# Optimization experiments

Hardware: AMD Instinct MI355X
Metric: run time of the kernel (lower is better)

Reference implementation:

```python
import jax, jax.numpy as jnp
import numpy as np

B, S, DM, H, SD = 8, 2048, 512, 8, 64
INNER = H * SD
HID = 4 * DM
EPS = 1e-5


def setup_inputs() -> dict:
    key = jax.random.key(0)
    ks = jax.random.split(key, 12)
    p = lambda k, sh: jax.random.normal(k, sh, dtype=jnp.float32) * 0.02
    return {
        "x": jax.random.normal(ks[0], (B, S, DM), dtype=jnp.float32),
        "norm_g": jnp.ones((DM,), jnp.float32),
        "norm_b": jnp.zeros((DM,), jnp.float32),
        "ffn_norm_g": jnp.ones((DM,), jnp.float32),
        "ffn_norm_b": jnp.zeros((DM,), jnp.float32),
        "Wa": p(ks[1], (INNER, DM)),
        "Wb": p(ks[2], (INNER, DM)),
        "Wql": p(ks[3], (INNER, DM)),
        "Wqr": p(ks[4], (INNER, DM)),
        "Wsd": p(ks[5], (H, DM)),
        "bsd": jnp.zeros((H,), jnp.float32),
        "Wpd": p(ks[6], (H, DM)),
        "bpd": jnp.zeros((H,), jnp.float32),
        "Wout": p(ks[7], (DM, INNER)),
        "W1": p(ks[8], (HID, DM)),
        "b1": jnp.zeros((HID,), jnp.float32),
        "W2": p(ks[9], (DM, HID)),
        "b2": jnp.zeros((DM,), jnp.float32),
    }


def _ln(x, g, b):
    m = x.mean(-1, keepdims=True)
    v = ((x - m) ** 2).mean(-1, keepdims=True)
    return (x - m) / jnp.sqrt(v + EPS) * g + b


def reference(x, norm_g, norm_b, ffn_norm_g, ffn_norm_b, Wa, Wb, Wql, Wqr,
              Wsd, bsd, Wpd, bpd, Wout, W1, b1, W2, b2):
    n = _ln(x, norm_g, norm_b)  # [B,S,DM]
    # project, reshape to heads, move time axis first for scan: [S,B,H,SD]
    tm = lambda t: t.reshape(B, S, H, SD).transpose(1, 0, 2, 3)
    a_all = tm(jnp.tanh(n @ Wa.T))
    b_all = tm(jnp.tanh(n @ Wb.T))
    ql_all = tm(jnp.tanh(n @ Wql.T))
    qr_all = tm(jnp.tanh(n @ Wqr.T))
    sd_all = jax.nn.sigmoid(n @ Wsd.T + bsd).transpose(1, 0, 2)[..., None]        # [S,B,H,1]
    pd_all = jax.nn.sigmoid(n @ Wpd.T + bpd).transpose(1, 0, 2)[..., None, None]  # [S,B,H,1,1]

    def step(carry, inp):
        state, pair = carry  # state [B,H,SD], pair [B,H,SD,SD]
        at, bt, qlt, sdt, pdt = inp
        prev = state
        state = sdt * state + (1.0 - sdt) * at
        pair = pdt * pair + (1.0 - pdt) * jnp.einsum('bhd,bhe->bhde', prev, bt)
        lc = jnp.einsum('bhde,bhd->bhe', pair, qlt)  # left context [B,H,SD]
        return (state, pair), lc

    init = (jnp.zeros((B, H, SD), x.dtype), jnp.zeros((B, H, SD, SD), x.dtype))
    _, lc = jax.lax.scan(step, init, (a_all, b_all, ql_all, sd_all, pd_all))  # [S,B,H,SD]

    mixed = ((lc * qr_all).transpose(1, 0, 2, 3).reshape(B, S, INNER)) @ Wout.T  # [B,S,DM]
    r = x + mixed  # dropout is identity in eval
    h = jax.nn.gelu(_ln(r, ffn_norm_g, ffn_norm_b) @ W1.T + b1, approximate=False)
    return r + h @ W2.T + b2
```

## Files before the change

kernel.cpp:

```cpp
#include <hip/hip_runtime.h>
#include <cstdint>
#include <cstddef>

#define B_    8
#define S_    2048
#define DM_   512
#define H_    8
#define SD_   64
#define HID_  2048
#define ROWS  (B_*S_)
#define BH    (B_*H_)
#define NCHUNK 32
#define CLEN   64
#define EPS_  1e-5f

typedef __bf16 bf16x8 __attribute__((ext_vector_type(8)));
typedef float  floatx4 __attribute__((ext_vector_type(4)));

static __device__ __forceinline__ float bf2f(unsigned short h){
  union { unsigned int u; float f; } v; v.u = ((unsigned int)h) << 16; return v.f;
}
static __device__ __forceinline__ unsigned short f2bf(float f){
  union { float f; unsigned int u; } v; v.f = f;
  unsigned int r = v.u + 0x7fffu + ((v.u >> 16) & 1u);
  return (unsigned short)(r >> 16);
}
static __device__ __forceinline__ float fast_tanh(float x){
  float ax = fabsf(x);
  float e  = __expf(2.f*ax);
  float t  = 1.f - 2.f/(e+1.f);
  return copysignf(t, x);
}
static __device__ __forceinline__ float sigmoidf_(float z){
  return 1.f/(1.f + expf(-z));
}
static __device__ __forceinline__ float gelu_exact(float x){
  return 0.5f*x*(1.f + erff(x*0.70710678118654752440f));
}
static __device__ __forceinline__ void gld_lds16(const unsigned short* g, unsigned short* lds){
  __builtin_amdgcn_global_load_lds(
      (const __attribute__((address_space(1))) void*)g,
      (__attribute__((address_space(3))) void*)lds,
      16, 0, 0);
}
static __device__ __forceinline__ int swz(int row, int col){
  return row*64 + (((col>>3) ^ (row&7))<<3) + (col&7);
}

__global__ __launch_bounds__(256) void cvt_weights(
    const float* __restrict__ wa, const float* __restrict__ wb,
    const float* __restrict__ wql, const float* __restrict__ wqr,
    const float* __restrict__ wout, const float* __restrict__ w1,
    const float* __restrict__ w2,
    unsigned short* __restrict__ wcat, unsigned short* __restrict__ woutb,
    unsigned short* __restrict__ w1b, unsigned short* __restrict__ w2b){
  int i = blockIdx.x*256 + threadIdx.x;
  const float* s; unsigned short* d; int base;
  if      (i <  65536){ s=wa;   d=wcat;          base=i; }
  else if (i < 131072){ s=wb;   d=wcat+262144;   base=i-65536; }
  else if (i < 196608){ s=wql;  d=wcat+524288;   base=i-131072; }
  else if (i < 262144){ s=wqr;  d=wcat+786432;   base=i-196608; }
  else if (i < 327680){ s=wout; d=woutb;         base=i-262144; }
  else if (i < 589824){ s=w1;   d=w1b;           base=i-327680; }
  else                { s=w2;   d=w2b;           base=i-589824; }
  float4 v = ((const float4*)s)[base];
  ushort4 o; o.x=f2bf(v.x); o.y=f2bf(v.y); o.z=f2bf(v.z); o.w=f2bf(v.w);
  ((ushort4*)d)[base] = o;
}

__global__ __launch_bounds__(64) void ln_gates(
    const float* __restrict__ x, const float* __restrict__ gam, const float* __restrict__ bet,
    const float* __restrict__ Wsd, const float* __restrict__ bsd,
    const float* __restrict__ Wpd, const float* __restrict__ bpd,
    unsigned short* __restrict__ nbf, float* __restrict__ sdo, float* __restrict__ pdo){
  const int row = blockIdx.x, l = threadIdx.x;
  const float* xr = x + (size_t)row*DM_;
  float4 v0 = ((const float4*)xr)[l*2];
  float4 v1 = ((const float4*)xr)[l*2+1];
  float v[8] = {v0.x,v0.y,v0.z,v0.w,v1.x,v1.y,v1.z,v1.w};
  float s = 0.f;
  #pragma unroll
  for (int i=0;i<8;++i) s += v[i];
  #pragma unroll
  for (int m=1;m<64;m<<=1) s += __shfl_xor(s, m);
  const float mean = s * (1.f/512.f);
  float q = 0.f;
  #pragma unroll
  for (int i=0;i<8;++i){ float d = v[i]-mean; q += d*d; }
  #pragma unroll
  for (int m=1;m<64;m<<=1) q += __shfl_xor(q, m);
  const float rstd = rsqrtf(q*(1.f/512.f) + EPS_);
  float4 g0 = ((const float4*)gam)[l*2], g1 = ((const float4*)gam)[l*2+1];
  float4 b0 = ((const float4*)bet)[l*2], b1 = ((const float4*)bet)[l*2+1];
  float gg[8] = {g0.x,g0.y,g0.z,g0.w,g1.x,g1.y,g1.z,g1.w};
  float bb[8] = {b0.x,b0.y,b0.z,b0.w,b1.x,b1.y,b1.z,b1.w};
  float n[8];
  #pragma unroll
  for (int i=0;i<8;++i) n[i] = (v[i]-mean)*rstd*gg[i] + bb[i];
  ushort4 o0, o1;
  o0.x=f2bf(n[0]); o0.y=f2bf(n[1]); o0.z=f2bf(n[2]); o0.w=f2bf(n[3]);
  o1.x=f2bf(n[4]); o1.y=f2bf(n[5]); o1.z=f2bf(n[6]); o1.w=f2bf(n[7]);
  ((ushort4*)(nbf + (size_t)row*DM_))[l*2]   = o0;
  ((ushort4*)(nbf + (size_t)row*DM_))[l*2+1] = o1;
  float acc[16];
  #pragma unroll
  for (int hh=0; hh<8; ++hh){
    const float4* ws = (const float4*)(Wsd + hh*DM_) + l*2;
    const float4* wp = (const float4*)(Wpd + hh*DM_) + l*2;
    float4 a0=ws[0], a1=ws[1], p0=wp[0], p1=wp[1];
    acc[hh]   = n[0]*a0.x+n[1]*a0.y+n[2]*a0.z+n[3]*a0.w+n[4]*a1.x+n[5]*a1.y+n[6]*a1.z+n[7]*a1.w;
    acc[8+hh] = n[0]*p0.x+n[1]*p0.y+n[2]*p0.z+n[3]*p0.w+n[4]*p1.x+n[5]*p1.y+n[6]*p1.z+n[7]*p1.w;
  }
  #pragma unroll
  for (int k=0;k<16;++k){
    float a = acc[k];
    #pragma unroll
    for (int m=1;m<64;m<<=1) a += __shfl_xor(a, m);
    acc[k] = a;
  }
  if (l==0){
    #pragma unroll
    for (int hh=0; hh<8; ++hh){
      sdo[row*8+hh] = sigmoidf_(acc[hh]   + bsd[hh]);
      pdo[row*8+hh] = sigmoidf_(acc[8+hh] + bpd[hh]);
    }
  }
}

__global__ __launch_bounds__(64) void ln_plain(
    const unsigned short* __restrict__ xb, const float* __restrict__ gam, const float* __restrict__ bet,
    unsigned short* __restrict__ ob){
  const int row = blockIdx.x, l = threadIdx.x;
  const unsigned short* xr = xb + (size_t)row*DM_ + l*8;
  ushort4 u0 = *(const ushort4*)xr;
  ushort4 u1 = *(const ushort4*)(xr+4);
  float v[8] = {bf2f(u0.x),bf2f(u0.y),bf2f(u0.z),bf2f(u0.w),
                bf2f(u1.x),bf2f(u1.y),bf2f(u1.z),bf2f(u1.w)};
  float s = 0.f;
  #pragma unroll
  for (int i=0;i<8;++i) s += v[i];
  #pragma unroll
  for (int m=1;m<64;m<<=1) s += __shfl_xor(s, m);
  const float mean = s * (1.f/512.f);
  float q = 0.f;
  #pragma unroll
  for (int i=0;i<8;++i){ float d = v[i]-mean; q += d*d; }
  #pragma unroll
  for (int m=1;m<64;m<<=1) q += __shfl_xor(q, m);
  const float rstd = rsqrtf(q*(1.f/512.f) + EPS_);
  float4 g0 = ((const float4*)gam)[l*2], g1 = ((const float4*)gam)[l*2+1];
  float4 b0 = ((const float4*)bet)[l*2], b1 = ((const float4*)bet)[l*2+1];
  float gg[8] = {g0.x,g0.y,g0.z,g0.w,g1.x,g1.y,g1.z,g1.w};
  float bb[8] = {b0.x,b0.y,b0.z,b0.w,b1.x,b1.y,b1.z,b1.w};
  ushort4 o0, o1;
  o0.x=f2bf((v[0]-mean)*rstd*gg[0]+bb[0]); o0.y=f2bf((v[1]-mean)*rstd*gg[1]+bb[1]);
  o0.z=f2bf((v[2]-mean)*rstd*gg[2]+bb[2]); o0.w=f2bf((v[3]-mean)*rstd*gg[3]+bb[3]);
  o1.x=f2bf((v[4]-mean)*rstd*gg[4]+bb[4]); o1.y=f2bf((v[5]-mean)*rstd*gg[5]+bb[5]);
  o1.z=f2bf((v[6]-mean)*rstd*gg[6]+bb[6]); o1.w=f2bf((v[7]-mean)*rstd*gg[7]+bb[7]);
  ((ushort4*)(ob + (size_t)row*DM_))[l*2]   = o0;
  ((ushort4*)(ob + (size_t)row*DM_))[l*2+1] = o1;
}

template<int MODE>
__global__ __launch_bounds__(256) void gemm128(
    const unsigned short* __restrict__ A, const unsigned short* __restrict__ W,
    const float* __restrict__ bias, const float* __restrict__ residf,
    const unsigned short* __restrict__ residb,
    float* __restrict__ outf, unsigned short* __restrict__ outb,
    int N, int K){
  __shared__ __align__(16) unsigned short As[128*64];
  __shared__ __align__(16) unsigned short Ws[128*64];
  const int tid  = threadIdx.x;
  const int w    = tid >> 6;
  const int lane = tid & 63;
  const int mblk = blockIdx.x, nblk = blockIdx.y;
  const int mrow = (w >> 1) * 64;
  const int ncol = (w & 1) * 64;
  const int fr = lane & 15, fq = lane >> 4;

  int srow[4], scol[4];
  #pragma unroll
  for (int q=0;q<4;++q){
    const int p = q*256 + w*64 + lane;
    srow[q] = p >> 3;
    scol[q] = ((p & 7) ^ (srow[q] & 7)) * 8;
  }

  floatx4 acc[4][4];
  #pragma unroll
  for (int i=0;i<4;++i)
    #pragma unroll
    for (int j=0;j<4;++j)
      acc[i][j] = (floatx4){0.f,0.f,0.f,0.f};

  for (int k0=0; k0<K; k0+=64){
    #pragma unroll
    for (int q=0;q<4;++q){
      gld_lds16(A + (size_t)(mblk*128 + srow[q])*K + k0 + scol[q], As + (q*256 + w*64)*8);
      gld_lds16(W + (size_t)(nblk*128 + srow[q])*K + k0 + scol[q], Ws + (q*256 + w*64)*8);
    }
    __syncthreads();
    #pragma unroll
    for (int kh=0;kh<2;++kh){
      bf16x8 af[4], bf[4];
      #pragma unroll
      for (int i=0;i<4;++i) af[i] = *(const bf16x8*)&As[swz(mrow + i*16 + fr, kh*32 + fq*8)];
      #pragma unroll
      for (int j=0;j<4;++j) bf[j] = *(const bf16x8*)&Ws[swz(ncol + j*16 + fr, kh*32 + fq*8)];
      #pragma unroll
      for (int i=0;i<4;++i)
        #pragma unroll
        for (int j=0;j<4;++j)
          acc[i][j] = __builtin_amdgcn_mfma_f32_16x16x32_bf16(af[i], bf[j], acc[i][j], 0, 0, 0);
    }
    __syncthreads();
  }

  #pragma unroll
  for (int i=0;i<4;++i){
    const int grow_base = mblk*128 + mrow + i*16 + fq*4;
    #pragma unroll
    for (int j=0;j<4;++j){
      const int gcol = nblk*128 + ncol + j*16 + fr;
      float bias_v = 0.f;
      if (MODE==2 || MODE==3) bias_v = bias[gcol];
      #pragma unroll
      for (int r=0;r<4;++r){
        const size_t o = (size_t)(grow_base + r)*N + gcol;
        float v = acc[i][j][r];
        if      (MODE==0) outb[o] = f2bf(fast_tanh(v));
        else if (MODE==1) outb[o] = f2bf(residf[o] + v);
        else if (MODE==2) outb[o] = f2bf(gelu_exact(v + bias_v));
        else              outf[o] = bf2f(residb[o]) + v + bias_v;
      }
    }
  }
}

template<int MODE>
__global__ __launch_bounds__(256) void gemm128db(
    const unsigned short* __restrict__ A, const unsigned short* __restrict__ W,
    unsigned short* __restrict__ outb, int N, int K){
  __shared__ __align__(16) unsigned short As[2][128*64];
  __shared__ __align__(16) unsigned short Ws[2][128*64];
  const int tid  = threadIdx.x;
  const int w    = tid >> 6;
  const int lane = tid & 63;
  const int mblk = blockIdx.x, nblk = blockIdx.y;
  const int mrow = (w >> 1) * 64;
  const int ncol = (w & 1) * 64;
  const int fr = lane & 15, fq = lane >> 4;

  int srow[4], scol[4];
  #pragma unroll
  for (int q=0;q<4;++q){
    const int p = q*256 + w*64 + lane;
    srow[q] = p >> 3;
    scol[q] = ((p & 7) ^ (srow[q] & 7)) * 8;
  }

  floatx4 acc[4][4];
  #pragma unroll
  for (int i=0;i<4;++i)
    #pragma unroll
    for (int j=0;j<4;++j)
      acc[i][j] = (floatx4){0.f,0.f,0.f,0.f};

  #pragma unroll
  for (int q=0;q<4;++q){
    gld_lds16(A + (size_t)(mblk*128 + srow[q])*K + scol[q], As[0] + (q*256 + w*64)*8);
    gld_lds16(W + (size_t)(nblk*128 + srow[q])*K + scol[q], Ws[0] + (q*256 + w*64)*8);
  }

  const int nk = K >> 6;
  for (int it=0; it<nk; ++it){
    const int cur = it & 1;
    __syncthreads();
    if (it+1 < nk){
      const int k1 = (it+1) << 6;
      #pragma unroll
      for (int q=0;q<4;++q){
        gld_lds16(A + (size_t)(mblk*128 + srow[q])*K + k1 + scol[q], As[1-cur] + (q*256 + w*64)*8);
        gld_lds16(W + (size_t)(nblk*128 + srow[q])*K + k1 + scol[q], Ws[1-cur] + (q*256 + w*64)*8);
      }
    }
    #pragma unroll
    for (int kh=0;kh<2;++kh){
      bf16x8 af[4], bf[4];
      #pragma unroll
      for (int i=0;i<4;++i) af[i] = *(const bf16x8*)&As[cur][swz(mrow + i*16 + fr, kh*32 + fq*8)];
      #pragma unroll
      for (int j=0;j<4;++j) bf[j] = *(const bf16x8*)&Ws[cur][swz(ncol + j*16 + fr, kh*32 + fq*8)];
      #pragma unroll
      for (int i=0;i<4;++i)
        #pragma unroll
        for (int j=0;j<4;++j)
          acc[i][j] = __builtin_amdgcn_mfma_f32_16x16x32_bf16(af[i], bf[j], acc[i][j], 0, 0, 0);
    }
  }

  #pragma unroll
  for (int i=0;i<4;++i){
    const int grow_base = mblk*128 + mrow + i*16 + fq*4;
    #pragma unroll
    for (int j=0;j<4;++j){
      const int gcol = nblk*128 + ncol + j*16 + fr;
      #pragma unroll
      for (int r=0;r<4;++r){
        const size_t o = (size_t)(grow_base + r)*N + gcol;
        outb[o] = f2bf(fast_tanh(acc[i][j][r]));
      }
    }
  }
}

__global__ __launch_bounds__(64) void state_local(
    const unsigned short* __restrict__ proj, const float* __restrict__ sdo,
    unsigned short* __restrict__ slocb, float* __restrict__ Sarr,
    float* __restrict__ sEnd){
  const int c = blockIdx.x, bh = blockIdx.y, b = bh>>3, h = bh&7, d = threadIdx.x;
  float s = 0.f, S = 1.f;
  const int t0 = c*CLEN;
  #pragma unroll 4
  for (int j=0;j<CLEN;++j){
    const int t = t0 + j;
    float a  = bf2f(proj[((size_t)(b*S_+t))*2048 + h*64 + d]);
    float sv = sdo[(b*S_+t)*8 + h];
    s = sv*s + (1.f-sv)*a;
    S *= sv;
    slocb[((size_t)bh*S_ + t)*64 + d] = f2bf(s);
    if (d==0) Sarr[bh*S_ + t] = S;
  }
  sEnd[((size_t)c*BH + bh)*64 + d] = s;
}

__global__ __launch_bounds__(64) void state_combine(
    const float* __restrict__ sEnd, const float* __restrict__ Sarr,
    float* __restrict__ sinit){
  const int bh = blockIdx.x, d = threadIdx.x;
  float acc = 0.f;
  for (int c=0;c<NCHUNK;++c){
    sinit[((size_t)c*BH + bh)*64 + d] = acc;
    const int te = c*CLEN + CLEN - 1;
    acc = Sarr[bh*S_ + te]*acc + sEnd[((size_t)c*BH + bh)*64 + d];
  }
}

__global__ __launch_bounds__(256) void prev_mat(
    const unsigned short* __restrict__ slocb, const float* __restrict__ Sarr,
    const float* __restrict__ sinit, unsigned short* __restrict__ prevb){
  const size_t idx = (size_t)blockIdx.x*256 + threadIdx.x;
  const int d  = (int)(idx & 63);
  const size_t bt = idx >> 6;
  const int t  = (int)(bt & (S_-1));
  const int bh = (int)(bt >> 11);
  const int c = t >> 6, j = t & 63;
  float init = sinit[((size_t)c*BH + bh)*64 + d];
  float p;
  if (j==0) p = init;
  else {
    const size_t pt = (size_t)bh*S_ + (t-1);
    p = Sarr[pt]*init + bf2f(slocb[pt*64 + d]);
  }
  prevb[idx] = f2bf(p);
}

__global__ __launch_bounds__(64) void pair_localm(
    const unsigned short* __restrict__ proj, const float* __restrict__ pdo,
    const unsigned short* __restrict__ prevb, float* __restrict__ pairbuf,
    float* __restrict__ Dprod){
  __shared__ __align__(16) unsigned short Bt[4096];
  __shared__ __align__(16) unsigned short Pt[4096];
  const int c=blockIdx.x, bh=blockIdx.y, b=bh>>3, h=bh&7, l=threadIdx.x;
  const int t = c*CLEN + l;
  float pd = pdo[(b*S_+t)*8 + h];
  float D = pd;
  #pragma unroll
  for (int m=1;m<64;m<<=1){ float o = __shfl_up(D, m); if (l>=m) D *= o; }
  const float Dend = __shfl(D, 63);
  const float cu = (Dend / D) * (1.f - pd);
  if (l==63) Dprod[c*BH+bh] = Dend;
  {
    const unsigned short* brow = proj  + ((size_t)(b*S_+t))*2048 + 512 + h*64;
    const unsigned short* prow = prevb + ((size_t)bh*S_ + t)*64;
    #pragma unroll
    for (int e8=0;e8<8;++e8){
      ushort4 u0 = *(const ushort4*)(brow + e8*8);
      ushort4 u1 = *(const ushort4*)(brow + e8*8 + 4);
      unsigned short vs[8] = {u0.x,u0.y,u0.z,u0.w,u1.x,u1.y,u1.z,u1.w};
      ushort4 p0 = *(const ushort4*)(prow + e8*8);
      ushort4 p1 = *(const ushort4*)(prow + e8*8 + 4);
      unsigned short ps[8] = {p0.x,p0.y,p0.z,p0.w,p1.x,p1.y,p1.z,p1.w};
      #pragma unroll
      for (int q=0;q<8;++q){
        const int r = e8*8+q;
        Bt[swz(r, l)] = f2bf(cu * bf2f(vs[q]));
        Pt[swz(r, l)] = ps[q];
      }
    }
  }
  __syncthreads();
  const int fr = l & 15, fq = l >> 4;
  floatx4 acc[4][4];
  #pragma unroll
  for (int i=0;i<4;++i)
    #pragma unroll
    for (int j=0;j<4;++j) acc[i][j] = (floatx4){0.f,0.f,0.f,0.f};
  #pragma unroll
  for (int kh=0;kh<2;++kh){
    bf16x8 af[4], bfr[4];
    #pragma unroll
    for (int i=0;i<4;++i) af[i]  = *(const bf16x8*)&Bt[swz(i*16+fr, kh*32+fq*8)];
    #pragma unroll
    for (int j=0;j<4;++j) bfr[j] = *(const bf16x8*)&Pt[swz(j*16+fr, kh*32+fq*8)];
    #pragma unroll
    for (int i=0;i<4;++i)
      #pragma unroll
      for (int j=0;j<4;++j)
        acc[i][j] = __builtin_amdgcn_mfma_f32_16x16x32_bf16(af[i], bfr[j], acc[i][j], 0, 0, 0);
  }
  float* outp = pairbuf + ((size_t)c*BH + bh)*4096;
  #pragma unroll
  for (int i=0;i<4;++i)
    #pragma unroll
    for (int j=0;j<4;++j)
      #pragma unroll
      for (int r=0;r<4;++r)
        outp[(i*16+fq*4+r)*64 + j*16+fr] = acc[i][j][r];
}

__global__ __launch_bounds__(256) void pair_combine(
    float* __restrict__ pairbuf, const float* __restrict__ Dprod){
  const int idx = blockIdx.x*256 + threadIdx.x;
  const int de = idx & 4095, bh = idx >> 12;
  float acc = 0.f;
  for (int c=0;c<NCHUNK;++c){
    const size_t o = ((size_t)c*BH + bh)*4096 + de;
    float loc = pairbuf[o];
    pairbuf[o] = acc;
    acc = Dprod[c*BH + bh]*acc + loc;
  }
}

__global__ __launch_bounds__(64) void pair_finalm(
    const unsigned short* __restrict__ proj, const float* __restrict__ pdo,
    const unsigned short* __restrict__ prevb, const float* __restrict__ pinit,
    unsigned short* __restrict__ lcqr){
  __shared__ __align__(16) unsigned short Bt[4096];
  __shared__ __align__(16) unsigned short Tb[4096];
  __shared__ __align__(16) float Dtl[64];
  __shared__ __align__(16) float cudl[64];
  const int c=blockIdx.x, bh=blockIdx.y, b=bh>>3, h=bh&7, l=threadIdx.x;
  const int t0 = c*CLEN;
  const int trow = t0 + l;
  float pd = pdo[(b*S_+trow)*8 + h];
  float D = pd;
  #pragma unroll
  for (int m=1;m<64;m<<=1){ float o = __shfl_up(D, m); if (l>=m) D *= o; }
  Dtl[l]  = D;
  cudl[l] = (1.f - pd) / D;
  {
    const unsigned short* brow = proj + ((size_t)(b*S_+trow))*2048 + 512 + h*64;
    #pragma unroll
    for (int e8=0;e8<8;++e8){
      ushort4 u0 = *(const ushort4*)(brow + e8*8);
      ushort4 u1 = *(const ushort4*)(brow + e8*8 + 4);
      unsigned short vs[8] = {u0.x,u0.y,u0.z,u0.w,u1.x,u1.y,u1.z,u1.w};
      #pragma unroll
      for (int q=0;q<8;++q) Bt[swz(e8*8+q, l)] = vs[q];
    }
  }
  __syncthreads();
  const int fr = l & 15, fq = l >> 4;
  bf16x8 qf[4][2], pf[4][2];
  #pragma unroll
  for (int i=0;i<4;++i)
    #pragma unroll
    for (int kh=0;kh<2;++kh){
      qf[i][kh] = *(const bf16x8*)(proj  + ((size_t)(b*S_ + t0 + i*16 + fr))*2048 + 1024 + h*64 + kh*32 + fq*8);
      pf[i][kh] = *(const bf16x8*)(prevb + ((size_t)(bh*S_ + t0 + i*16 + fr))*64  + kh*32 + fq*8);
    }
  floatx4 sacc[4][4];
  #pragma unroll
  for (int i=0;i<4;++i)
    #pragma unroll
    for (int j=0;j<4;++j) sacc[i][j] = (floatx4){0.f,0.f,0.f,0.f};
  #pragma unroll
  for (int kh=0;kh<2;++kh)
    #pragma unroll
    for (int i=0;i<4;++i)
      #pragma unroll
      for (int j=0;j<4;++j)
        sacc[i][j] = __builtin_amdgcn_mfma_f32_16x16x32_bf16(qf[i][kh], pf[j][kh], sacc[i][j], 0, 0, 0);
  float mycud[4];
  #pragma unroll
  for (int j=0;j<4;++j) mycud[j] = cudl[j*16+fr];
  #pragma unroll
  for (int i=0;i<4;++i){
    floatx4 dtv = *(const floatx4*)&Dtl[i*16+fq*4];
    #pragma unroll
    for (int j=0;j<4;++j){
      const int uu = j*16+fr;
      #pragma unroll
      for (int r=0;r<4;++r){
        const int tt = i*16+fq*4+r;
        float v = (uu<=tt) ? (sacc[i][j][r]*dtv[r])*mycud[j] : 0.f;
        Tb[swz(tt, uu)] = f2bf(v);
      }
    }
  }
  __syncthreads();
  floatx4 acc[4][4];
  #pragma unroll
  for (int i=0;i<4;++i)
    #pragma unroll
    for (int j=0;j<4;++j) acc[i][j] = (floatx4){0.f,0.f,0.f,0.f};
  #pragma unroll
  for (int kh=0;kh<2;++kh){
    bf16x8 af[4], bfr[4];
    #pragma unroll
    for (int i=0;i<4;++i) af[i]  = *(const bf16x8*)&Tb[swz(i*16+fr, kh*32+fq*8)];
    #pragma unroll
    for (int j=0;j<4;++j) bfr[j] = *(const bf16x8*)&Bt[swz(j*16+fr, kh*32+fq*8)];
    #pragma unroll
    for (int i=0;i<4;++i)
      #pragma unroll
      for (int j=0;j<4;++j)
        acc[i][j] = __builtin_amdgcn_mfma_f32_16x16x32_bf16(af[i], bfr[j], acc[i][j], 0, 0, 0);
  }
  {
    const float* ibase = pinit + ((size_t)c*BH + bh)*4096;
    #pragma unroll
    for (int kh=0;kh<2;++kh){
      bf16x8 qs[4], inf[4];
      #pragma unroll
      for (int i=0;i<4;++i){
        const float sc = Dtl[i*16+fr];
        #pragma unroll
        for (int e=0;e<8;++e) qs[i][e] = (__bf16)(sc * (float)qf[i][kh][e]);
      }
      #pragma unroll
      for (int j=0;j<4;++j){
        const float* ip = ibase + (j*16+fr)*64 + kh*32 + fq*8;
        float4 f0 = *(const float4*)ip;
        float4 f1 = *(const float4*)(ip+4);
        inf[j][0]=(__bf16)f0.x; inf[j][1]=(__bf16)f0.y; inf[j][2]=(__bf16)f0.z; inf[j][3]=(__bf16)f0.w;
        inf[j][4]=(__bf16)f1.x; inf[j][5]=(__bf16)f1.y; inf[j][6]=(__bf16)f1.z; inf[j][7]=(__bf16)f1.w;
      }
      #pragma unroll
      for (int i=0;i<4;++i)
        #pragma unroll
        for (int j=0;j<4;++j)
          acc[i][j] = __builtin_amdgcn_mfma_f32_16x16x32_bf16(qs[i], inf[j], acc[i][j], 0, 0, 0);
    }
  }
  __syncthreads();
  #pragma unroll
  for (int i=0;i<4;++i)
    #pragma unroll
    for (int j=0;j<4;++j)
      #pragma unroll
      for (int r=0;r<4;++r)
        Tb[swz(i*16+fq*4+r, j*16+fr)] = f2bf(acc[i][j][r]);
  __syncthreads();
  {
    const unsigned short* qrow = proj + ((size_t)(b*S_+trow))*2048 + 1536 + h*64;
    unsigned short* orow = lcqr + ((size_t)(b*S_+trow))*512 + h*64;
    #pragma unroll
    for (int e8=0;e8<8;++e8){
      bf16x8 lcv = *(const bf16x8*)&Tb[swz(l, e8*8)];
      ushort4 q0 = *(const ushort4*)(qrow + e8*8);
      ushort4 q1 = *(const ushort4*)(qrow + e8*8 + 4);
      unsigned short qv[8] = {q0.x,q0.y,q0.z,q0.w,q1.x,q1.y,q1.z,q1.w};
      ushort4 o0, o1;
      o0.x = f2bf((float)lcv[0]*bf2f(qv[0]));
      o0.y = f2bf((float)lcv[1]*bf2f(qv[1]));
      o0.z = f2bf((float)lcv[2]*bf2f(qv[2]));
      o0.w = f2bf((float)lcv[3]*bf2f(qv[3]));
      o1.x = f2bf((float)lcv[4]*bf2f(qv[4]));
      o1.y = f2bf((float)lcv[5]*bf2f(qv[5]));
      o1.z = f2bf((float)lcv[6]*bf2f(qv[6]));
      o1.w = f2bf((float)lcv[7]*bf2f(qv[7]));
      *(ushort4*)(orow + e8*8)     = o0;
      *(ushort4*)(orow + e8*8 + 4) = o1;
    }
  }
}

extern "C" void kernel_launch(void* const* d_in, const int* in_sizes, int n_in,
                              void* d_out, int out_size, void* d_ws, size_t ws_size,
                              hipStream_t stream){
  (void)in_sizes; (void)n_in; (void)out_size; (void)ws_size;
  const float* x    = (const float*)d_in[0];
  const float* ng   = (const float*)d_in[1];
  const float* nb   = (const float*)d_in[2];
  const float* fng  = (const float*)d_in[3];
  const float* fnb  = (const float*)d_in[4];
  const float* Wa   = (const float*)d_in[5];
  const float* Wb   = (const float*)d_in[6];
  const float* Wql  = (const float*)d_in[7];
  const float* Wqr  = (const float*)d_in[8];
  const float* Wsd  = (const float*)d_in[9];
  const float* bsd  = (const float*)d_in[10];
  const float* Wpd  = (const float*)d_in[11];
  const float* bpd  = (const float*)d_in[12];
  const float* Wout = (const float*)d_in[13];
  const float* W1   = (const float*)d_in[14];
  const float* b1   = (const float*)d_in[15];
  const float* W2   = (const float*)d_in[16];
  const float* b2   = (const float*)d_in[17];
  float* out = (float*)d_out;
  char* ws = (char*)d_ws;

  size_t off = 0;
  auto alloc = [&](size_t bytes)->char*{ char* p = ws + off; off += (bytes + 255) & ~(size_t)255; return p; };
  char* RA = alloc((size_t)ROWS*DM_*2);
  char* RB = alloc((size_t)ROWS*2048*2);
  char* RD = alloc((size_t)BH*S_*64*4);
  char* RE = alloc((size_t)BH*S_*64*4);
  float* sdo   = (float*)alloc((size_t)ROWS*8*4);
  float* pdo   = (float*)alloc((size_t)ROWS*8*4);
  float* Sarr  = (float*)alloc((size_t)BH*S_*4);
  float* sinit = (float*)alloc((size_t)NCHUNK*BH*64*4);
  float* sEnd  = (float*)alloc((size_t)NCHUNK*BH*64*4);
  float* dprod = (float*)alloc((size_t)NCHUNK*BH*4);
  unsigned short* wcat  = (unsigned short*)alloc((size_t)2048*512*2);
  unsigned short* woutb = (unsigned short*)alloc((size_t)512*512*2);
  unsigned short* w1b   = (unsigned short*)alloc((size_t)2048*512*2);
  unsigned short* w2b   = (unsigned short*)alloc((size_t)512*2048*2);

  unsigned short* nbf   = (unsigned short*)RA;
  unsigned short* lcqr  = (unsigned short*)RA;
  unsigned short* nr    = (unsigned short*)RA;
  unsigned short* proj  = (unsigned short*)RB;
  unsigned short* hbuf  = (unsigned short*)RB;
  unsigned short* slocb = (unsigned short*)RD;
  float* pairb = (float*)RD;
  unsigned short* prevb = (unsigned short*)RE;
  unsigned short* rbufb = (unsigned short*)RE;

  cvt_weights<<<dim3(3328), dim3(256), 0, stream>>>(Wa,Wb,Wql,Wqr,Wout,W1,W2, wcat,woutb,w1b,w2b);
  ln_gates<<<dim3(ROWS), dim3(64), 0, stream>>>(x, ng, nb, Wsd, bsd, Wpd, bpd, nbf, sdo, pdo);
  gemm128db<0><<<dim3(128,16), dim3(256), 0, stream>>>(nbf, wcat, proj, 2048, 512);
  state_local<<<dim3(NCHUNK,BH), dim3(64), 0, stream>>>(proj, sdo, slocb, Sarr, sEnd);
  state_combine<<<dim3(BH), dim3(64), 0, stream>>>(sEnd, Sarr, sinit);
  prev_mat<<<dim3(32768), dim3(256), 0, stream>>>(slocb, Sarr, sinit, prevb);
  pair_localm<<<dim3(NCHUNK,BH), dim3(64), 0, stream>>>(proj, pdo, prevb, pairb, dprod);
  pair_combine<<<dim3(1024), dim3(256), 0, stream>>>(pairb, dprod);
  pair_finalm<<<dim3(NCHUNK,BH), dim3(64), 0, stream>>>(proj, pdo, prevb, pairb, lcqr);
  gemm128<1><<<dim3(128,4), dim3(256), 0, stream>>>(lcqr, woutb, nullptr, x, nullptr, nullptr, rbufb, 512, 512);
  ln_plain<<<dim3(ROWS), dim3(64), 0, stream>>>(rbufb, fng, fnb, nr);
  gemm128<2><<<dim3(128,16), dim3(256), 0, stream>>>(nr, w1b, b1, nullptr, nullptr, nullptr, hbuf, 2048, 512);
  gemm128<3><<<dim3(128,4), dim3(256), 0, stream>>>(hbuf, w2b, b2, nullptr, rbufb, out, nullptr, 512, 2048);
}
```

Baseline: 441.2 us.

## Use 256x256-tile 8-wave GEMM for projection and FFN-up layers

Replaces the 128x128 double-buffered GEMM with a 256x256-tile, 512-thread kernel for the combined projection GEMM and the W1 GEMM. It also adds explicit vmcnt/lgkmcnt waits, s_barrier interleaving, sched barriers and setprio around the MFMA phases, with loads issued two tiles ahead. The larger tile raises arithmetic intensity and LDS reuse. In exchange it uses 128 KB of LDS per block and fewer blocks (512), which lowers occupancy and wave parallelism.

```diff
diff --git a/kernel.cpp b/kernel.cpp
--- a/kernel.cpp
+++ b/kernel.cpp
@@ -238,77 +238,161 @@
 }
 
 template<int MODE>
-__global__ __launch_bounds__(256) void gemm128db(
+__global__ __launch_bounds__(512, 2) void gemm256(
     const unsigned short* __restrict__ A, const unsigned short* __restrict__ W,
-    unsigned short* __restrict__ outb, int N, int K){
-  __shared__ __align__(16) unsigned short As[2][128*64];
-  __shared__ __align__(16) unsigned short Ws[2][128*64];
+    const float* __restrict__ bias, unsigned short* __restrict__ outb,
+    int N, int K){
+  __shared__ __align__(16) unsigned short lds[65536];
   const int tid  = threadIdx.x;
   const int w    = tid >> 6;
   const int lane = tid & 63;
+  const int mrow = (w >> 2) * 128;
+  const int ncol = (w & 3) * 64;
+  const int fr   = lane & 15, fq = lane >> 4;
   const int mblk = blockIdx.x, nblk = blockIdx.y;
-  const int mrow = (w >> 1) * 64;
-  const int ncol = (w & 1) * 64;
-  const int fr = lane & 15, fq = lane >> 4;
+  const int nt   = K >> 6;
 
   int srow[4], scol[4];
   #pragma unroll
   for (int q=0;q<4;++q){
-    const int p = q*256 + w*64 + lane;
+    const int p = q*512 + tid;
     srow[q] = p >> 3;
-    scol[q] = ((p & 7) ^ (srow[q] & 7)) * 8;
-  }
-
-  floatx4 acc[4][4];
-  #pragma unroll
-  for (int i=0;i<4;++i)
-    #pragma unroll
-    for (int j=0;j<4;++j)
-      acc[i][j] = (floatx4){0.f,0.f,0.f,0.f};
+    scol[q] = (((p & 7) ^ (srow[q] & 7)) << 3);
+  }
+  const unsigned short* Ag = A + (size_t)(mblk*256)*K;
+  const unsigned short* Wg = W + (size_t)(nblk*256)*K;
+
+  const int sx0 = ((fq    ) ^ (fr & 7)) << 3;
+  const int sx1 = ((4 + fq) ^ (fr & 7)) << 3;
+
+  floatx4 acc[8][4];
+  #pragma unroll
+  for (int i=0;i<8;++i)
+    #pragma unroll
+    for (int j=0;j<4;++j) acc[i][j] = (floatx4){0.f,0.f,0.f,0.f};
 
   #pragma unroll
   for (int q=0;q<4;++q){
-    gld_lds16(A + (size_t)(mblk*128 + srow[q])*K + scol[q], As[0] + (q*256 + w*64)*8);
-    gld_lds16(W + (size_t)(nblk*128 + srow[q])*K + scol[q], Ws[0] + (q*256 + w*64)*8);
-  }
-
-  const int nk = K >> 6;
-  for (int it=0; it<nk; ++it){
-    const int cur = it & 1;
-    __syncthreads();
-    if (it+1 < nk){
-      const int k1 = (it+1) << 6;
+    gld_lds16(Ag + (size_t)srow[q]*K + scol[q],      lds +         (q*512 + w*64)*8);
+    gld_lds16(Wg + (size_t)srow[q]*K + scol[q],      lds + 16384 + (q*512 + w*64)*8);
+  }
+  #pragma unroll
+  for (int q=0;q<4;++q){
+    gld_lds16(Ag + (size_t)srow[q]*K + 64 + scol[q], lds + 32768 + (q*512 + w*64)*8);
+    gld_lds16(Wg + (size_t)srow[q]*K + 64 + scol[q], lds + 49152 + (q*512 + w*64)*8);
+  }
+
+  bf16x8 bfr[2][2][2];
+  for (int t=0; t<nt; ++t){
+    unsigned short* As = lds + ((t & 1) << 15);
+    unsigned short* Ws = As + 16384;
+
+    if (t == nt-1) asm volatile("s_waitcnt vmcnt(0)" ::: "memory");
+    else           asm volatile("s_waitcnt vmcnt(8)" ::: "memory");
+    __builtin_amdgcn_s_barrier();
+
+    bf16x8 af[4][2];
+
+    #pragma unroll
+    for (int ii=0;ii<4;++ii){
+      const int rb = (mrow + ii*16 + fr)*64;
+      af[ii][0] = *(const bf16x8*)&As[rb + sx0];
+      af[ii][1] = *(const bf16x8*)&As[rb + sx1];
+    }
+    #pragma unroll
+    for (int jj=0;jj<2;++jj){
+      const int rb = (ncol + jj*16 + fr)*64;
+      bfr[0][jj][0] = *(const bf16x8*)&Ws[rb + sx0];
+      bfr[0][jj][1] = *(const bf16x8*)&Ws[rb + sx1];
+    }
+    __builtin_amdgcn_s_barrier();
+    asm volatile("s_waitcnt lgkmcnt(0)" ::: "memory");
+    __builtin_amdgcn_sched_barrier(0);
+    __builtin_amdgcn_s_setprio(1);
+    #pragma unroll
+    for (int kh=0;kh<2;++kh)
+      #pragma unroll
+      for (int ii=0;ii<4;++ii)
+        #pragma unroll
+        for (int jj=0;jj<2;++jj)
+          acc[ii][jj] = __builtin_amdgcn_mfma_f32_16x16x32_bf16(af[ii][kh], bfr[0][jj][kh], acc[ii][jj], 0, 0, 0);
+    __builtin_amdgcn_s_setprio(0);
+    __builtin_amdgcn_s_barrier();
+
+    #pragma unroll
+    for (int jj=0;jj<2;++jj){
+      const int rb = (ncol + (2+jj)*16 + fr)*64;
+      bfr[1][jj][0] = *(const bf16x8*)&Ws[rb + sx0];
+      bfr[1][jj][1] = *(const bf16x8*)&Ws[rb + sx1];
+    }
+    __builtin_amdgcn_s_barrier();
+    asm volatile("s_waitcnt lgkmcnt(0)" ::: "memory");
+    __builtin_amdgcn_sched_barrier(0);
+    __builtin_amdgcn_s_setprio(1);
+    #pragma unroll
+    for (int kh=0;kh<2;++kh)
+      #pragma unroll
+      for (int ii=0;ii<4;++ii)
+        #pragma unroll
+        for (int jj=0;jj<2;++jj)
+          acc[ii][2+jj] = __builtin_amdgcn_mfma_f32_16x16x32_bf16(af[ii][kh], bfr[1][jj][kh], acc[ii][2+jj], 0, 0, 0);
+    __builtin_amdgcn_s_setprio(0);
+    __builtin_amdgcn_s_barrier();
+
+    #pragma unroll
+    for (int ii=0;ii<4;++ii){
+      const int rb = (mrow + 64 + ii*16 + fr)*64;
+      af[ii][0] = *(const bf16x8*)&As[rb + sx0];
+      af[ii][1] = *(const bf16x8*)&As[rb + sx1];
+    }
+    __builtin_amdgcn_s_barrier();
+    asm volatile("s_waitcnt lgkmcnt(0)" ::: "memory");
+    __builtin_amdgcn_sched_barrier(0);
+    __builtin_amdgcn_s_setprio(1);
+    #pragma unroll
+    for (int kh=0;kh<2;++kh)
+      #pragma unroll
+      for (int ii=0;ii<4;++ii)
+        #pragma unroll
+        for (int jj=0;jj<2;++jj)
+          acc[4+ii][jj] = __builtin_amdgcn_mfma_f32_16x16x32_bf16(af[ii][kh], bfr[0][jj][kh], acc[4+ii][jj], 0, 0, 0);
+    __builtin_amdgcn_s_setprio(0);
+    __builtin_amdgcn_s_barrier();
+
+    if (t + 2 < nt){
+      const int k2 = (t + 2) << 6;
       #pragma unroll
       for (int q=0;q<4;++q){
-        gld_lds16(A + (size_t)(mblk*128 + srow[q])*K + k1 + scol[q], As[1-cur] + (q*256 + w*64)*8);
-        gld_lds16(W + (size_t)(nblk*128 + srow[q])*K + k1 + scol[q], Ws[1-cur] + (q*256 + w*64)*8);
+        gld_lds16(Ag + (size_t)srow[q]*K + k2 + scol[q], As + (q*512 + w*64)*8);
+        gld_lds16(Wg + (size_t)srow[q]*K + k2 + scol[q], Ws + (q*512 + w*64)*8);
       }
     }
-    #pragma unroll
-    for (int kh=0;kh<2;++kh){
-      bf16x8 af[4], bf[4];
-      #pragma unroll
-      for (int i=0;i<4;++i) af[i] = *(const bf16x8*)&As[cur][swz(mrow + i*16 + fr, kh*32 + fq*8)];
-      #pragma unroll
-      for (int j=0;j<4;++j) bf[j] = *(const bf16x8*)&Ws[cur][swz(ncol + j*16 + fr, kh*32 + fq*8)];
-      #pragma unroll
-      for (int i=0;i<4;++i)
+
+    __builtin_amdgcn_s_setprio(1);
+    #pragma unroll
+    for (int kh=0;kh<2;++kh)
+      #pragma unroll
+      for (int ii=0;ii<4;++ii)
         #pragma unroll
-        for (int j=0;j<4;++j)
-          acc[i][j] = __builtin_amdgcn_mfma_f32_16x16x32_bf16(af[i], bf[j], acc[i][j], 0, 0, 0);
-    }
-  }
-
-  #pragma unroll
-  for (int i=0;i<4;++i){
-    const int grow_base = mblk*128 + mrow + i*16 + fq*4;
+        for (int jj=0;jj<2;++jj)
+          acc[4+ii][2+jj] = __builtin_amdgcn_mfma_f32_16x16x32_bf16(af[ii][kh], bfr[1][jj][kh], acc[4+ii][2+jj], 0, 0, 0);
+    __builtin_amdgcn_s_setprio(0);
+  }
+
+  #pragma unroll
+  for (int i=0;i<8;++i){
+    const int grow0 = mblk*256 + mrow + i*16 + fq*4;
     #pragma unroll
     for (int j=0;j<4;++j){
-      const int gcol = nblk*128 + ncol + j*16 + fr;
+      const int gcol = nblk*256 + ncol + j*16 + fr;
+      float bias_v = 0.f;
+      if (MODE==2) bias_v = bias[gcol];
       #pragma unroll
       for (int r=0;r<4;++r){
-        const size_t o = (size_t)(grow_base + r)*N + gcol;
-        outb[o] = f2bf(fast_tanh(acc[i][j][r]));
+        const size_t o = (size_t)(grow0 + r)*N + gcol;
+        float v = acc[i][j][r];
+        if (MODE==0) outb[o] = f2bf(fast_tanh(v));
+        else         outb[o] = f2bf(gelu_exact(v + bias_v));
       }
     }
   }
@@ -641,7 +725,7 @@
 
   cvt_weights<<<dim3(3328), dim3(256), 0, stream>>>(Wa,Wb,Wql,Wqr,Wout,W1,W2, wcat,woutb,w1b,w2b);
   ln_gates<<<dim3(ROWS), dim3(64), 0, stream>>>(x, ng, nb, Wsd, bsd, Wpd, bpd, nbf, sdo, pdo);
-  gemm128db<0><<<dim3(128,16), dim3(256), 0, stream>>>(nbf, wcat, proj, 2048, 512);
+  gemm256<0><<<dim3(64,8), dim3(512), 0, stream>>>(nbf, wcat, nullptr, proj, 2048, 512);
   state_local<<<dim3(NCHUNK,BH), dim3(64), 0, stream>>>(proj, sdo, slocb, Sarr, sEnd);
   state_combine<<<dim3(BH), dim3(64), 0, stream>>>(sEnd, Sarr, sinit);
   prev_mat<<<dim3(32768), dim3(256), 0, stream>>>(slocb, Sarr, sinit, prevb);
@@ -650,6 +734,6 @@
   pair_finalm<<<dim3(NCHUNK,BH), dim3(64), 0, stream>>>(proj, pdo, prevb, pairb, lcqr);
   gemm128<1><<<dim3(128,4), dim3(256), 0, stream>>>(lcqr, woutb, nullptr, x, nullptr, nullptr, rbufb, 512, 512);
   ln_plain<<<dim3(ROWS), dim3(64), 0, stream>>>(rbufb, fng, fnb, nr);
-  gemm128<2><<<dim3(128,16), dim3(256), 0, stream>>>(nr, w1b, b1, nullptr, nullptr, nullptr, hbuf, 2048, 512);
+  gemm256<2><<<dim3(64,8), dim3(512), 0, stream>>>(nr, w1b, b1, hbuf, 2048, 512);
   gemm128<3><<<dim3(128,4), dim3(256), 0, stream>>>(hbuf, w2b, b2, nullptr, rbufb, out, nullptr, 512, 2048);
 }
```

Result: no change. 440.9 us (-0.1%).

## Fuse prev-state reconstruction into pair kernels, store pair init in bf16

Applied to the files above, without the earlier changes.

Drops the prev_mat kernel and rebuilds the previous state on the fly inside pair_localm and pair_finalm from slocb, Sarr and sinit. pair_combine now writes chunk-initial pair states to a separate bf16 buffer, so pair_finalm reads half the bytes. Also packs four rows per block in the two layernorm kernels and replaces the double-buffered projection GEMM with the single-buffer gemm128. Buffers are remapped, and the pair workspace region is enlarged to hold chunk pair states.

```diff
diff --git a/kernel.cpp b/kernel.cpp
--- a/kernel.cpp
+++ b/kernel.cpp
@@ -68,12 +68,12 @@
   ((ushort4*)d)[base] = o;
 }
 
-__global__ __launch_bounds__(64) void ln_gates(
+__global__ __launch_bounds__(256) void ln_gates(
     const float* __restrict__ x, const float* __restrict__ gam, const float* __restrict__ bet,
     const float* __restrict__ Wsd, const float* __restrict__ bsd,
     const float* __restrict__ Wpd, const float* __restrict__ bpd,
     unsigned short* __restrict__ nbf, float* __restrict__ sdo, float* __restrict__ pdo){
-  const int row = blockIdx.x, l = threadIdx.x;
+  const int row = blockIdx.x*4 + (threadIdx.x>>6), l = threadIdx.x & 63;
   const float* xr = x + (size_t)row*DM_;
   float4 v0 = ((const float4*)xr)[l*2];
   float4 v1 = ((const float4*)xr)[l*2+1];
@@ -127,10 +127,10 @@
   }
 }
 
-__global__ __launch_bounds__(64) void ln_plain(
+__global__ __launch_bounds__(256) void ln_plain(
     const unsigned short* __restrict__ xb, const float* __restrict__ gam, const float* __restrict__ bet,
     unsigned short* __restrict__ ob){
-  const int row = blockIdx.x, l = threadIdx.x;
+  const int row = blockIdx.x*4 + (threadIdx.x>>6), l = threadIdx.x & 63;
   const unsigned short* xr = xb + (size_t)row*DM_ + l*8;
   ushort4 u0 = *(const ushort4*)xr;
   ushort4 u1 = *(const ushort4*)(xr+4);
@@ -237,83 +237,6 @@
   }
 }
 
-template<int MODE>
-__global__ __launch_bounds__(256) void gemm128db(
-    const unsigned short* __restrict__ A, const unsigned short* __restrict__ W,
-    unsigned short* __restrict__ outb, int N, int K){
-  __shared__ __align__(16) unsigned short As[2][128*64];
-  __shared__ __align__(16) unsigned short Ws[2][128*64];
-  const int tid  = threadIdx.x;
-  const int w    = tid >> 6;
-  const int lane = tid & 63;
-  const int mblk = blockIdx.x, nblk = blockIdx.y;
-  const int mrow = (w >> 1) * 64;
-  const int ncol = (w & 1) * 64;
-  const int fr = lane & 15, fq = lane >> 4;
-
-  int srow[4], scol[4];
-  #pragma unroll
-  for (int q=0;q<4;++q){
-    const int p = q*256 + w*64 + lane;
-    srow[q] = p >> 3;
-    scol[q] = ((p & 7) ^ (srow[q] & 7)) * 8;
-  }
-
-  floatx4 acc[4][4];
-  #pragma unroll
-  for (int i=0;i<4;++i)
-    #pragma unroll
-    for (int j=0;j<4;++j)
-      acc[i][j] = (floatx4){0.f,0.f,0.f,0.f};
-
-  #pragma unroll
-  for (int q=0;q<4;++q){
-    gld_lds16(A + (size_t)(mblk*128 + srow[q])*K + scol[q], As[0] + (q*256 + w*64)*8);
-    gld_lds16(W + (size_t)(nblk*128 + srow[q])*K + scol[q], Ws[0] + (q*256 + w*64)*8);
-  }
-
-  const int nk = K >> 6;
-  for (int it=0; it<nk; ++it){
-    const int cur = it & 1;
-    __syncthreads();
-    if (it+1 < nk){
-      const int k1 = (it+1) << 6;
-      #pragma unroll
-      for (int q=0;q<4;++q){
-        gld_lds16(A + (size_t)(mblk*128 + srow[q])*K + k1 + scol[q], As[1-cur] + (q*256 + w*64)*8);
-        gld_lds16(W + (size_t)(nblk*128 + srow[q])*K + k1 + scol[q], Ws[1-cur] + (q*256 + w*64)*8);
-      }
-    }
-    #pragma unroll
-    for (int kh=0;kh<2;++kh){
-      bf16x8 af[4], bf[4];
-      #pragma unroll
-      for (int i=0;i<4;++i) af[i] = *(const bf16x8*)&As[cur][swz(mrow + i*16 + fr, kh*32 + fq*8)];
-      #pragma unroll
-      for (int j=0;j<4;++j) bf[j] = *(const bf16x8*)&Ws[cur][swz(ncol + j*16 + fr, kh*32 + fq*8)];
-      #pragma unroll
-      for (int i=0;i<4;++i)
-        #pragma unroll
-        for (int j=0;j<4;++j)
-          acc[i][j] = __builtin_amdgcn_mfma_f32_16x16x32_bf16(af[i], bf[j], acc[i][j], 0, 0, 0);
-    }
-  }
-
-  #pragma unroll
-  for (int i=0;i<4;++i){
-    const int grow_base = mblk*128 + mrow + i*16 + fq*4;
-    #pragma unroll
-    for (int j=0;j<4;++j){
-      const int gcol = nblk*128 + ncol + j*16 + fr;
-      #pragma unroll
-      for (int r=0;r<4;++r){
-        const size_t o = (size_t)(grow_base + r)*N + gcol;
-        outb[o] = f2bf(fast_tanh(acc[i][j][r]));
-      }
-    }
-  }
-}
-
 __global__ __launch_bounds__(64) void state_local(
     const unsigned short* __restrict__ proj, const float* __restrict__ sdo,
     unsigned short* __restrict__ slocb, float* __restrict__ Sarr,
@@ -346,28 +269,10 @@
   }
 }
 
-__global__ __launch_bounds__(256) void prev_mat(
-    const unsigned short* __restrict__ slocb, const float* __restrict__ Sarr,
-    const float* __restrict__ sinit, unsigned short* __restrict__ prevb){
-  const size_t idx = (size_t)blockIdx.x*256 + threadIdx.x;
-  const int d  = (int)(idx & 63);
-  const size_t bt = idx >> 6;
-  const int t  = (int)(bt & (S_-1));
-  const int bh = (int)(bt >> 11);
-  const int c = t >> 6, j = t & 63;
-  float init = sinit[((size_t)c*BH + bh)*64 + d];
-  float p;
-  if (j==0) p = init;
-  else {
-    const size_t pt = (size_t)bh*S_ + (t-1);
-    p = Sarr[pt]*init + bf2f(slocb[pt*64 + d]);
-  }
-  prevb[idx] = f2bf(p);
-}
-
 __global__ __launch_bounds__(64) void pair_localm(
     const unsigned short* __restrict__ proj, const float* __restrict__ pdo,
-    const unsigned short* __restrict__ prevb, float* __restrict__ pairbuf,
+    const unsigned short* __restrict__ slocb, const float* __restrict__ Sarr,
+    const float* __restrict__ sinit, float* __restrict__ pairbuf,
     float* __restrict__ Dprod){
   __shared__ __align__(16) unsigned short Bt[4096];
   __shared__ __align__(16) unsigned short Pt[4096];
@@ -382,20 +287,28 @@
   if (l==63) Dprod[c*BH+bh] = Dend;
   {
     const unsigned short* brow = proj  + ((size_t)(b*S_+t))*2048 + 512 + h*64;
-    const unsigned short* prow = prevb + ((size_t)bh*S_ + t)*64;
+    const size_t ptm = (size_t)bh*S_ + (l==0 ? t : t-1);
+    const unsigned short* srow = slocb + ptm*64;
+    const float* initp = sinit + ((size_t)c*BH + bh)*64;
+    float sp = 0.f;
+    if (l>0) sp = Sarr[ptm];
     #pragma unroll
     for (int e8=0;e8<8;++e8){
       ushort4 u0 = *(const ushort4*)(brow + e8*8);
       ushort4 u1 = *(const ushort4*)(brow + e8*8 + 4);
       unsigned short vs[8] = {u0.x,u0.y,u0.z,u0.w,u1.x,u1.y,u1.z,u1.w};
-      ushort4 p0 = *(const ushort4*)(prow + e8*8);
-      ushort4 p1 = *(const ushort4*)(prow + e8*8 + 4);
-      unsigned short ps[8] = {p0.x,p0.y,p0.z,p0.w,p1.x,p1.y,p1.z,p1.w};
+      ushort4 s0 = *(const ushort4*)(srow + e8*8);
+      ushort4 s1 = *(const ushort4*)(srow + e8*8 + 4);
+      unsigned short ss[8] = {s0.x,s0.y,s0.z,s0.w,s1.x,s1.y,s1.z,s1.w};
+      float4 i0 = *(const float4*)(initp + e8*8);
+      float4 i1 = *(const float4*)(initp + e8*8 + 4);
+      float iv[8] = {i0.x,i0.y,i0.z,i0.w,i1.x,i1.y,i1.z,i1.w};
       #pragma unroll
       for (int q=0;q<8;++q){
         const int r = e8*8+q;
+        float p = (l==0) ? iv[q] : (sp*iv[q] + bf2f(ss[q]));
         Bt[swz(r, l)] = f2bf(cu * bf2f(vs[q]));
-        Pt[swz(r, l)] = ps[q];
+        Pt[swz(r, l)] = f2bf(p);
       }
     }
   }
@@ -430,21 +343,22 @@
 }
 
 __global__ __launch_bounds__(256) void pair_combine(
-    float* __restrict__ pairbuf, const float* __restrict__ Dprod){
+    const float* __restrict__ pairbuf, const float* __restrict__ Dprod,
+    unsigned short* __restrict__ pinitb){
   const int idx = blockIdx.x*256 + threadIdx.x;
   const int de = idx & 4095, bh = idx >> 12;
   float acc = 0.f;
   for (int c=0;c<NCHUNK;++c){
     const size_t o = ((size_t)c*BH + bh)*4096 + de;
-    float loc = pairbuf[o];
-    pairbuf[o] = acc;
-    acc = Dprod[c*BH + bh]*acc + loc;
+    pinitb[o] = f2bf(acc);
+    acc = Dprod[c*BH + bh]*acc + pairbuf[o];
   }
 }
 
 __global__ __launch_bounds__(64) void pair_finalm(
     const unsigned short* __restrict__ proj, const float* __restrict__ pdo,
-    const unsigned short* __restrict__ prevb, const float* __restrict__ pinit,
+    const unsigned short* __restrict__ slocb, const float* __restrict__ Sarr,
+    const float* __restrict__ sinit, const unsigned short* __restrict__ pinitb,
     unsigned short* __restrict__ lcqr){
   __shared__ __align__(16) unsigned short Bt[4096];
   __shared__ __align__(16) unsigned short Tb[4096];
@@ -472,14 +386,31 @@
   }
   __syncthreads();
   const int fr = l & 15, fq = l >> 4;
+  const float* initp = sinit + ((size_t)c*BH + bh)*64;
   bf16x8 qf[4][2], pf[4][2];
   #pragma unroll
-  for (int i=0;i<4;++i)
+  for (int i=0;i<4;++i){
+    const int tr = t0 + i*16 + fr;
+    const bool first = (i==0 && fr==0);
+    const size_t ptm = (size_t)bh*S_ + (first ? tr : tr-1);
+    float sp = 0.f;
+    if (!first) sp = Sarr[ptm];
     #pragma unroll
     for (int kh=0;kh<2;++kh){
-      qf[i][kh] = *(const bf16x8*)(proj  + ((size_t)(b*S_ + t0 + i*16 + fr))*2048 + 1024 + h*64 + kh*32 + fq*8);
-      pf[i][kh] = *(const bf16x8*)(prevb + ((size_t)(bh*S_ + t0 + i*16 + fr))*64  + kh*32 + fq*8);
-    }
+      qf[i][kh] = *(const bf16x8*)(proj + ((size_t)(b*S_ + tr))*2048 + 1024 + h*64 + kh*32 + fq*8);
+      bf16x8 sv = *(const bf16x8*)(slocb + ptm*64 + kh*32 + fq*8);
+      float4 i0 = *(const float4*)(initp + kh*32 + fq*8);
+      float4 i1 = *(const float4*)(initp + kh*32 + fq*8 + 4);
+      float iv[8] = {i0.x,i0.y,i0.z,i0.w,i1.x,i1.y,i1.z,i1.w};
+      bf16x8 pv;
+      #pragma unroll
+      for (int e=0;e<8;++e){
+        float p = first ? iv[e] : (sp*iv[e] + (float)sv[e]);
+        pv[e] = (__bf16)p;
+      }
+      pf[i][kh] = pv;
+    }
+  }
   floatx4 sacc[4][4];
   #pragma unroll
   for (int i=0;i<4;++i)
@@ -529,7 +460,7 @@
         acc[i][j] = __builtin_amdgcn_mfma_f32_16x16x32_bf16(af[i], bfr[j], acc[i][j], 0, 0, 0);
   }
   {
-    const float* ibase = pinit + ((size_t)c*BH + bh)*4096;
+    const unsigned short* ib = pinitb + ((size_t)c*BH + bh)*4096;
     #pragma unroll
     for (int kh=0;kh<2;++kh){
       bf16x8 qs[4], inf[4];
@@ -540,13 +471,8 @@
         for (int e=0;e<8;++e) qs[i][e] = (__bf16)(sc * (float)qf[i][kh][e]);
       }
       #pragma unroll
-      for (int j=0;j<4;++j){
-        const float* ip = ibase + (j*16+fr)*64 + kh*32 + fq*8;
-        float4 f0 = *(const float4*)ip;
-        float4 f1 = *(const float4*)(ip+4);
-        inf[j][0]=(__bf16)f0.x; inf[j][1]=(__bf16)f0.y; inf[j][2]=(__bf16)f0.z; inf[j][3]=(__bf16)f0.w;
-        inf[j][4]=(__bf16)f1.x; inf[j][5]=(__bf16)f1.y; inf[j][6]=(__bf16)f1.z; inf[j][7]=(__bf16)f1.w;
-      }
+      for (int j=0;j<4;++j)
+        inf[j] = *(const bf16x8*)(ib + (j*16+fr)*64 + kh*32 + fq*8);
       #pragma unroll
       for (int i=0;i<4;++i)
         #pragma unroll
@@ -616,7 +542,7 @@
   auto alloc = [&](size_t bytes)->char*{ char* p = ws + off; off += (bytes + 255) & ~(size_t)255; return p; };
   char* RA = alloc((size_t)ROWS*DM_*2);
   char* RB = alloc((size_t)ROWS*2048*2);
-  char* RD = alloc((size_t)BH*S_*64*4);
+  char* RD = alloc((size_t)NCHUNK*BH*4096*4);
   char* RE = alloc((size_t)BH*S_*64*4);
   float* sdo   = (float*)alloc((size_t)ROWS*8*4);
   float* pdo   = (float*)alloc((size_t)ROWS*8*4);
@@ -634,22 +560,21 @@
   unsigned short* nr    = (unsigned short*)RA;
   unsigned short* proj  = (unsigned short*)RB;
   unsigned short* hbuf  = (unsigned short*)RB;
-  unsigned short* slocb = (unsigned short*)RD;
   float* pairb = (float*)RD;
-  unsigned short* prevb = (unsigned short*)RE;
-  unsigned short* rbufb = (unsigned short*)RE;
+  unsigned short* slocb  = (unsigned short*)RE;
+  unsigned short* rbufb  = (unsigned short*)RE;
+  unsigned short* pinitb = (unsigned short*)(RE + (size_t)BH*S_*64*2);
 
   cvt_weights<<<dim3(3328), dim3(256), 0, stream>>>(Wa,Wb,Wql,Wqr,Wout,W1,W2, wcat,woutb,w1b,w2b);
-  ln_gates<<<dim3(ROWS), dim3(64), 0, stream>>>(x, ng, nb, Wsd, bsd, Wpd, bpd, nbf, sdo, pdo);
-  gemm128db<0><<<dim3(128,16), dim3(256), 0, stream>>>(nbf, wcat, proj, 2048, 512);
+  ln_gates<<<dim3(ROWS/4), dim3(256), 0, stream>>>(x, ng, nb, Wsd, bsd, Wpd, bpd, nbf, sdo, pdo);
+  gemm128<0><<<dim3(128,16), dim3(256), 0, stream>>>(nbf, wcat, nullptr, nullptr, nullptr, nullptr, proj, 2048, 512);
   state_local<<<dim3(NCHUNK,BH), dim3(64), 0, stream>>>(proj, sdo, slocb, Sarr, sEnd);
   state_combine<<<dim3(BH), dim3(64), 0, stream>>>(sEnd, Sarr, sinit);
-  prev_mat<<<dim3(32768), dim3(256), 0, stream>>>(slocb, Sarr, sinit, prevb);
-  pair_localm<<<dim3(NCHUNK,BH), dim3(64), 0, stream>>>(proj, pdo, prevb, pairb, dprod);
-  pair_combine<<<dim3(1024), dim3(256), 0, stream>>>(pairb, dprod);
-  pair_finalm<<<dim3(NCHUNK,BH), dim3(64), 0, stream>>>(proj, pdo, prevb, pairb, lcqr);
+  pair_localm<<<dim3(NCHUNK,BH), dim3(64), 0, stream>>>(proj, pdo, slocb, Sarr, sinit, pairb, dprod);
+  pair_combine<<<dim3(1024), dim3(256), 0, stream>>>(pairb, dprod, pinitb);
+  pair_finalm<<<dim3(NCHUNK,BH), dim3(64), 0, stream>>>(proj, pdo, slocb, Sarr, sinit, pinitb, lcqr);
   gemm128<1><<<dim3(128,4), dim3(256), 0, stream>>>(lcqr, woutb, nullptr, x, nullptr, nullptr, rbufb, 512, 512);
-  ln_plain<<<dim3(ROWS), dim3(64), 0, stream>>>(rbufb, fng, fnb, nr);
+  ln_plain<<<dim3(ROWS/4), dim3(256), 0, stream>>>(rbufb, fng, fnb, nr);
   gemm128<2><<<dim3(128,16), dim3(256), 0, stream>>>(nr, w1b, b1, nullptr, nullptr, nullptr, hbuf, 2048, 512);
   gemm128<3><<<dim3(128,4), dim3(256), 0, stream>>>(hbuf, w2b, b2, nullptr, rbufb, out, nullptr, 512, 2048);
 }
```

Result: faster. 425.1 us (-3.6%).
